# Kernel optimization log

Hardware: AMD Instinct MI355X
Metric: run time of the kernel (lower is better)

Reference implementation:

```python
import jax, jax.numpy as jnp
import numpy as np

N, E = 20000, 200000
DIM, EDGE_DIM, HID = 128, 64, 256


def _linear_init(key, fan_in, fan_out):
    # torch nn.Linear default: U(-1/sqrt(fan_in), 1/sqrt(fan_in)) for W and b
    kw, kb = jax.random.split(key)
    bound = 1.0 / np.sqrt(fan_in)
    W = jax.random.uniform(kw, (fan_in, fan_out), minval=-bound, maxval=bound, dtype=jnp.float32)
    b = jax.random.uniform(kb, (fan_out,), minval=-bound, maxval=bound, dtype=jnp.float32)
    return W, b


def setup_inputs() -> dict:
    key = jax.random.key(0)
    ks = jax.random.split(key, 8)
    H = jax.random.normal(ks[0], (N, DIM), dtype=jnp.float32)
    src = jax.random.randint(ks[1], (E,), 0, N, dtype=jnp.int32)
    dst = jax.random.randint(ks[2], (E,), 0, N, dtype=jnp.int32)
    edge_index = jnp.stack([src, dst], axis=0)
    edge_attr = jax.random.normal(ks[3], (E, EDGE_DIM), dtype=jnp.float32)
    msg_W1, msg_b1 = _linear_init(ks[4], DIM + EDGE_DIM, HID)
    msg_W2, msg_b2 = _linear_init(ks[5], HID, DIM)
    self_W1, self_b1 = _linear_init(ks[6], DIM, HID)
    self_W2, self_b2 = _linear_init(ks[7], HID, DIM)
    eps = jnp.zeros((1,), dtype=jnp.float32)
    return dict(H=H, edge_index=edge_index, edge_attr=edge_attr, eps=eps,
                msg_W1=msg_W1, msg_b1=msg_b1, msg_W2=msg_W2, msg_b2=msg_b2,
                self_W1=self_W1, self_b1=self_b1, self_W2=self_W2, self_b2=self_b2)


def _mlp(x, W1, b1, W2, b2):
    h = jax.nn.relu(x @ W1 + b1)
    return h @ W2 + b2


def reference(H, edge_index, edge_attr, eps,
              msg_W1, msg_b1, msg_W2, msg_b2,
              self_W1, self_b1, self_W2, self_b2):
    src, dst = edge_index[0], edge_index[1]
    # gather source node features, concat edge features -> per-edge message MLP
    msg_in = jnp.concatenate([H[src], edge_attr], axis=-1)  # [E, dim+edge_dim]
    msg = _mlp(msg_in, msg_W1, msg_b1, msg_W2, msg_b2)       # [E, dim]
    # scatter-add messages to destination nodes
    agg = jax.ops.segment_sum(msg, dst, num_segments=H.shape[0])  # [N, dim]
    return _mlp((1.0 + eps) * H + agg, self_W1, self_b1, self_W2, self_b2)
```

## Files before the change

kernel.cpp:

```cpp
#include <hip/hip_runtime.h>

typedef float  f32x4  __attribute__((ext_vector_type(4)));
typedef short  bf16x8 __attribute__((ext_vector_type(8)));
typedef unsigned short u16;

#define NN   20000
#define NE   200000
#define DIM  128
#define EDIM 64
#define HID  256
#define KIN  192

__device__ __forceinline__ u16 f2b(float f) {
  unsigned u = __float_as_uint(f);
  u += 0x7FFFu + ((u >> 16) & 1u);
  return (u16)(u >> 16);
}

__global__ void prep_kernel(const float* __restrict__ mW1, const float* __restrict__ mW2,
                            const float* __restrict__ sW1, const float* __restrict__ sW2,
                            u16* __restrict__ W1T, u16* __restrict__ W2T,
                            u16* __restrict__ S1T, u16* __restrict__ S2T) {
  int t  = blockIdx.x * blockDim.x + threadIdx.x;
  int nt = gridDim.x * blockDim.x;
  for (int i = t; i < KIN * HID; i += nt) { int k = i / HID, n = i % HID; W1T[n * KIN + k] = f2b(mW1[i]); }
  for (int i = t; i < HID * DIM; i += nt) { int k = i / DIM, n = i % DIM; W2T[n * HID + k] = f2b(mW2[i]); }
  for (int i = t; i < DIM * HID; i += nt) { int k = i / HID, n = i % HID; S1T[n * DIM + k] = f2b(sW1[i]); }
  for (int i = t; i < HID * DIM; i += nt) { int k = i / DIM, n = i % DIM; S2T[n * HID + k] = f2b(sW2[i]); }
}

__global__ __launch_bounds__(256) void edge_kernel(
    const float* __restrict__ H, const int* __restrict__ EI,
    const float* __restrict__ EA,
    const u16* __restrict__ W1T, const float* __restrict__ b1p,
    const u16* __restrict__ W2T, const float* __restrict__ b2p,
    float* __restrict__ agg) {
  __shared__ int src_s[64];
  __shared__ int dst_s[64];
  __shared__ u16 smem[64 * HID];

  const int tid = threadIdx.x;
  const int e0  = blockIdx.x * 64;
  if (tid < 64)       src_s[tid]      = EI[e0 + tid];
  else if (tid < 128) dst_s[tid - 64] = EI[NE + e0 + tid - 64];
  __syncthreads();

  #pragma unroll
  for (int i = 0; i < 8; ++i) {
    int idx = tid + i * 256;
    int row = idx >> 5, c4 = idx & 31;
    const float4 v = reinterpret_cast<const float4*>(H + (size_t)src_s[row] * DIM)[c4];
    int by = (c4 * 8) ^ ((row & 7) << 4);
    ushort4 o; o.x = f2b(v.x); o.y = f2b(v.y); o.z = f2b(v.z); o.w = f2b(v.w);
    *reinterpret_cast<ushort4*>(&smem[row * KIN + (by >> 1)]) = o;
  }
  #pragma unroll
  for (int i = 0; i < 4; ++i) {
    int idx = tid + i * 256;
    int row = idx >> 4, c4 = idx & 15;
    const float4 v = reinterpret_cast<const float4*>(EA + (size_t)(e0 + row) * EDIM)[c4];
    int by = (256 + c4 * 8) ^ ((row & 7) << 4);
    ushort4 o; o.x = f2b(v.x); o.y = f2b(v.y); o.z = f2b(v.z); o.w = f2b(v.w);
    *reinterpret_cast<ushort4*>(&smem[row * KIN + (by >> 1)]) = o;
  }
  __syncthreads();

  const int wv = tid >> 6, lane = tid & 63;
  const int lr = lane & 15, lg = lane >> 4;
  const f32x4 zero = {0.f, 0.f, 0.f, 0.f};

  const int n0 = wv * 64;
  f32x4 acc[4][4];
  #pragma unroll
  for (int m = 0; m < 4; ++m)
    #pragma unroll
    for (int n = 0; n < 4; ++n) acc[m][n] = zero;
  float bias1[4];
  #pragma unroll
  for (int n = 0; n < 4; ++n) bias1[n] = b1p[n0 + n * 16 + lr];

  #pragma unroll
  for (int kt = 0; kt < 6; ++kt) {
    bf16x8 af[4], bf[4];
    #pragma unroll
    for (int m = 0; m < 4; ++m) {
      int row = m * 16 + lr;
      int by  = (kt * 64 + lg * 16) ^ ((row & 7) << 4);
      af[m] = *reinterpret_cast<const bf16x8*>(&smem[row * KIN + (by >> 1)]);
    }
    #pragma unroll
    for (int n = 0; n < 4; ++n) {
      int nabs = n0 + n * 16 + lr;
      bf[n] = *reinterpret_cast<const bf16x8*>(&W1T[nabs * KIN + kt * 32 + lg * 8]);
    }
    #pragma unroll
    for (int m = 0; m < 4; ++m)
      #pragma unroll
      for (int n = 0; n < 4; ++n)
        acc[m][n] = __builtin_amdgcn_mfma_f32_16x16x32_bf16(af[m], bf[n], acc[m][n], 0, 0, 0);
  }
  __syncthreads();

  #pragma unroll
  for (int m = 0; m < 4; ++m)
    #pragma unroll
    for (int n = 0; n < 4; ++n)
      #pragma unroll
      for (int r = 0; r < 4; ++r) {
        int row = m * 16 + lg * 4 + r;
        int col = n0 + n * 16 + lr;
        float v = acc[m][n][r] + bias1[n];
        v = fmaxf(v, 0.0f);
        int by = (col * 2) ^ ((row & 7) << 4);
        smem[row * HID + (by >> 1)] = f2b(v);
      }
  __syncthreads();

  const int n0b = wv * 32;
  f32x4 acc2[4][2];
  #pragma unroll
  for (int m = 0; m < 4; ++m) { acc2[m][0] = zero; acc2[m][1] = zero; }
  float bias2[2];
  #pragma unroll
  for (int n = 0; n < 2; ++n) bias2[n] = b2p[n0b + n * 16 + lr];

  #pragma unroll
  for (int kt = 0; kt < 8; ++kt) {
    bf16x8 af[4], bf[2];
    #pragma unroll
    for (int m = 0; m < 4; ++m) {
      int row = m * 16 + lr;
      int by  = (kt * 64 + lg * 16) ^ ((row & 7) << 4);
      af[m] = *reinterpret_cast<const bf16x8*>(&smem[row * HID + (by >> 1)]);
    }
    #pragma unroll
    for (int n = 0; n < 2; ++n) {
      int nabs = n0b + n * 16 + lr;
      bf[n] = *reinterpret_cast<const bf16x8*>(&W2T[nabs * HID + kt * 32 + lg * 8]);
    }
    #pragma unroll
    for (int m = 0; m < 4; ++m)
      #pragma unroll
      for (int n = 0; n < 2; ++n)
        acc2[m][n] = __builtin_amdgcn_mfma_f32_16x16x32_bf16(af[m], bf[n], acc2[m][n], 0, 0, 0);
  }

  #pragma unroll
  for (int m = 0; m < 4; ++m)
    #pragma unroll
    for (int n = 0; n < 2; ++n) {
      int col = n0b + n * 16 + lr;
      float bb = bias2[n];
      #pragma unroll
      for (int r = 0; r < 4; ++r) {
        int row = m * 16 + lg * 4 + r;
        int d   = dst_s[row];
        atomicAdd(&agg[(size_t)d * DIM + col], acc2[m][n][r] + bb);
      }
    }
}

__global__ __launch_bounds__(256) void self_kernel(
    const float* __restrict__ H, const float* __restrict__ agg,
    const float* __restrict__ epsp,
    const u16* __restrict__ S1T, const float* __restrict__ b1p,
    const u16* __restrict__ S2T, const float* __restrict__ b2p,
    float* __restrict__ out) {
  __shared__ u16 smem[64 * HID];
  const int tid = threadIdx.x;
  const int r0  = blockIdx.x * 64;
  const float sc = 1.0f + epsp[0];

  #pragma unroll
  for (int i = 0; i < 8; ++i) {
    int idx = tid + i * 256;
    int row = idx >> 5, c4 = idx & 31;
    int gr = r0 + row; gr = gr < NN ? gr : NN - 1;
    const float4 h = reinterpret_cast<const float4*>(H   + (size_t)gr * DIM)[c4];
    const float4 a = reinterpret_cast<const float4*>(agg + (size_t)gr * DIM)[c4];
    ushort4 o;
    o.x = f2b(sc * h.x + a.x); o.y = f2b(sc * h.y + a.y);
    o.z = f2b(sc * h.z + a.z); o.w = f2b(sc * h.w + a.w);
    int by = (c4 * 8) ^ ((row & 7) << 4);
    *reinterpret_cast<ushort4*>(&smem[row * DIM + (by >> 1)]) = o;
  }
  __syncthreads();

  const int wv = tid >> 6, lane = tid & 63;
  const int lr = lane & 15, lg = lane >> 4;
  const f32x4 zero = {0.f, 0.f, 0.f, 0.f};

  const int n0 = wv * 64;
  f32x4 acc[4][4];
  #pragma unroll
  for (int m = 0; m < 4; ++m)
    #pragma unroll
    for (int n = 0; n < 4; ++n) acc[m][n] = zero;
  float bias1[4];
  #pragma unroll
  for (int n = 0; n < 4; ++n) bias1[n] = b1p[n0 + n * 16 + lr];

  #pragma unroll
  for (int kt = 0; kt < 4; ++kt) {
    bf16x8 af[4], bf[4];
    #pragma unroll
    for (int m = 0; m < 4; ++m) {
      int row = m * 16 + lr;
      int by  = (kt * 64 + lg * 16) ^ ((row & 7) << 4);
      af[m] = *reinterpret_cast<const bf16x8*>(&smem[row * DIM + (by >> 1)]);
    }
    #pragma unroll
    for (int n = 0; n < 4; ++n) {
      int nabs = n0 + n * 16 + lr;
      bf[n] = *reinterpret_cast<const bf16x8*>(&S1T[nabs * DIM + kt * 32 + lg * 8]);
    }
    #pragma unroll
    for (int m = 0; m < 4; ++m)
      #pragma unroll
      for (int n = 0; n < 4; ++n)
        acc[m][n] = __builtin_amdgcn_mfma_f32_16x16x32_bf16(af[m], bf[n], acc[m][n], 0, 0, 0);
  }
  __syncthreads();

  #pragma unroll
  for (int m = 0; m < 4; ++m)
    #pragma unroll
    for (int n = 0; n < 4; ++n)
      #pragma unroll
      for (int r = 0; r < 4; ++r) {
        int row = m * 16 + lg * 4 + r;
        int col = n0 + n * 16 + lr;
        float v = acc[m][n][r] + bias1[n];
        v = fmaxf(v, 0.0f);
        int by = (col * 2) ^ ((row & 7) << 4);
        smem[row * HID + (by >> 1)] = f2b(v);
      }
  __syncthreads();

  const int n0b = wv * 32;
  f32x4 acc2[4][2];
  #pragma unroll
  for (int m = 0; m < 4; ++m) { acc2[m][0] = zero; acc2[m][1] = zero; }
  float bias2[2];
  #pragma unroll
  for (int n = 0; n < 2; ++n) bias2[n] = b2p[n0b + n * 16 + lr];

  #pragma unroll
  for (int kt = 0; kt < 8; ++kt) {
    bf16x8 af[4], bf[2];
    #pragma unroll
    for (int m = 0; m < 4; ++m) {
      int row = m * 16 + lr;
      int by  = (kt * 64 + lg * 16) ^ ((row & 7) << 4);
      af[m] = *reinterpret_cast<const bf16x8*>(&smem[row * HID + (by >> 1)]);
    }
    #pragma unroll
    for (int n = 0; n < 2; ++n) {
      int nabs = n0b + n * 16 + lr;
      bf[n] = *reinterpret_cast<const bf16x8*>(&S2T[nabs * HID + kt * 32 + lg * 8]);
    }
    #pragma unroll
    for (int m = 0; m < 4; ++m)
      #pragma unroll
      for (int n = 0; n < 2; ++n)
        acc2[m][n] = __builtin_amdgcn_mfma_f32_16x16x32_bf16(af[m], bf[n], acc2[m][n], 0, 0, 0);
  }

  #pragma unroll
  for (int m = 0; m < 4; ++m)
    #pragma unroll
    for (int n = 0; n < 2; ++n) {
      int col = n0b + n * 16 + lr;
      float bb = bias2[n];
      #pragma unroll
      for (int r = 0; r < 4; ++r) {
        int row = m * 16 + lg * 4 + r;
        int gr  = r0 + row;
        if (gr < NN) out[(size_t)gr * DIM + col] = acc2[m][n][r] + bb;
      }
    }
}

extern "C" void kernel_launch(void* const* d_in, const int* in_sizes, int n_in,
                              void* d_out, int out_size, void* d_ws, size_t ws_size,
                              hipStream_t stream) {
  const float* H   = (const float*)d_in[0];
  const int*   EI  = (const int*)  d_in[1];
  const float* EA  = (const float*)d_in[2];
  const float* EPS = (const float*)d_in[3];
  const float* mW1 = (const float*)d_in[4];
  const float* mb1 = (const float*)d_in[5];
  const float* mW2 = (const float*)d_in[6];
  const float* mb2 = (const float*)d_in[7];
  const float* sW1 = (const float*)d_in[8];
  const float* sb1 = (const float*)d_in[9];
  const float* sW2 = (const float*)d_in[10];
  const float* sb2 = (const float*)d_in[11];
  float* out = (float*)d_out;

  char* ws = (char*)d_ws;
  float* agg = (float*)ws;
  size_t off = (size_t)NN * DIM * 4;
  u16* W1T = (u16*)(ws + off); off += (size_t)HID * KIN * 2;
  u16* W2T = (u16*)(ws + off); off += (size_t)DIM * HID * 2;
  u16* S1T = (u16*)(ws + off); off += (size_t)HID * DIM * 2;
  u16* S2T = (u16*)(ws + off); off += (size_t)DIM * HID * 2;

  hipMemsetAsync(agg, 0, (size_t)NN * DIM * 4, stream);
  prep_kernel<<<96, 256, 0, stream>>>(mW1, mW2, sW1, sW2, W1T, W2T, S1T, S2T);
  edge_kernel<<<NE / 64, 256, 0, stream>>>(H, EI, EA, W1T, mb1, W2T, mb2, agg);
  self_kernel<<<(NN + 63) / 64, 256, 0, stream>>>(H, agg, EPS, S1T, sb1, S2T, sb2, out);
}
```

Before: 244.5 us.

## Replace float atomic scatter with CSR-sorted bf16 messages and gather reduction

Builds a per-destination histogram and prefix scan so that each edge message gets a slot in a dst-sorted buffer. The edge kernel now writes bf16 messages into that buffer instead of issuing fp32 atomicAdds to agg. A new node kernel reduces each node's contiguous messages before running the self MLP, using 32-row tiles. This removes the 25.6M global float atomics and the agg memset. In exchange it adds two small kernels (one of them a single-block scan), a 51MB message buffer, and bf16 rounding of each message before summation.

```diff
diff --git a/kernel.cpp b/kernel.cpp
--- a/kernel.cpp
+++ b/kernel.cpp
@@ -15,6 +15,9 @@
   unsigned u = __float_as_uint(f);
   u += 0x7FFFu + ((u >> 16) & 1u);
   return (u16)(u >> 16);
+}
+__device__ __forceinline__ float b2f(u16 v) {
+  return __uint_as_float(((unsigned)v) << 16);
 }
 
 __global__ void prep_kernel(const float* __restrict__ mW1, const float* __restrict__ mW2,
@@ -29,20 +32,58 @@
   for (int i = t; i < HID * DIM; i += nt) { int k = i / DIM, n = i % DIM; S2T[n * HID + k] = f2b(sW2[i]); }
 }
 
-__global__ __launch_bounds__(256) void edge_kernel(
+__global__ void hist_kernel(const int* __restrict__ EI, int* __restrict__ cnt) {
+  int i = blockIdx.x * 256 + threadIdx.x;
+  if (i < NE) atomicAdd(&cnt[EI[NE + i]], 1);
+}
+
+__global__ __launch_bounds__(1024) void scan_kernel(const int* __restrict__ cnt,
+                                                    int* __restrict__ start,
+                                                    int* __restrict__ cursor) {
+  __shared__ int ls[1024];
+  const int t = threadIdx.x;
+  const int base = t * 20;
+  int v[20]; int s = 0;
+  #pragma unroll
+  for (int j = 0; j < 20; ++j) {
+    int idx = base + j;
+    int c = (idx < NN) ? cnt[idx] : 0;
+    v[j] = s; s += c;
+  }
+  ls[t] = s;
+  __syncthreads();
+  for (int off = 1; off < 1024; off <<= 1) {
+    int x = (t >= off) ? ls[t - off] : 0;
+    __syncthreads();
+    ls[t] += x;
+    __syncthreads();
+  }
+  int boff = (t > 0) ? ls[t - 1] : 0;
+  #pragma unroll
+  for (int j = 0; j < 20; ++j) {
+    int idx = base + j;
+    if (idx < NN) { int val = boff + v[j]; start[idx] = val; cursor[idx] = val; }
+  }
+  if (t == 0) start[NN] = NE;
+}
+
+__global__ __launch_bounds__(256, 4) void edge_kernel(
     const float* __restrict__ H, const int* __restrict__ EI,
     const float* __restrict__ EA,
     const u16* __restrict__ W1T, const float* __restrict__ b1p,
     const u16* __restrict__ W2T, const float* __restrict__ b2p,
-    float* __restrict__ agg) {
+    int* __restrict__ cursor, u16* __restrict__ msg) {
   __shared__ int src_s[64];
-  __shared__ int dst_s[64];
+  __shared__ int pos_s[64];
   __shared__ u16 smem[64 * HID];
 
   const int tid = threadIdx.x;
   const int e0  = blockIdx.x * 64;
-  if (tid < 64)       src_s[tid]      = EI[e0 + tid];
-  else if (tid < 128) dst_s[tid - 64] = EI[NE + e0 + tid - 64];
+  if (tid < 64) {
+    int e = e0 + tid;
+    src_s[tid] = EI[e];
+    pos_s[tid] = atomicAdd(&cursor[EI[NE + e]], 1);
+  }
   __syncthreads();
 
   #pragma unroll
@@ -154,35 +195,57 @@
       #pragma unroll
       for (int r = 0; r < 4; ++r) {
         int row = m * 16 + lg * 4 + r;
-        int d   = dst_s[row];
-        atomicAdd(&agg[(size_t)d * DIM + col], acc2[m][n][r] + bb);
-      }
-    }
-}
-
-__global__ __launch_bounds__(256) void self_kernel(
-    const float* __restrict__ H, const float* __restrict__ agg,
-    const float* __restrict__ epsp,
+        msg[(size_t)pos_s[row] * DIM + col] = f2b(acc2[m][n][r] + bb);
+      }
+    }
+}
+
+__global__ __launch_bounds__(256, 6) void node_kernel(
+    const float* __restrict__ H, const u16* __restrict__ msg,
+    const int* __restrict__ start_g, const float* __restrict__ epsp,
     const u16* __restrict__ S1T, const float* __restrict__ b1p,
     const u16* __restrict__ S2T, const float* __restrict__ b2p,
     float* __restrict__ out) {
-  __shared__ u16 smem[64 * HID];
+  __shared__ int start_s[33];
+  __shared__ u16 smem[32 * HID];
   const int tid = threadIdx.x;
-  const int r0  = blockIdx.x * 64;
+  const int r0  = blockIdx.x * 32;
   const float sc = 1.0f + epsp[0];
 
-  #pragma unroll
-  for (int i = 0; i < 8; ++i) {
-    int idx = tid + i * 256;
-    int row = idx >> 5, c4 = idx & 31;
-    int gr = r0 + row; gr = gr < NN ? gr : NN - 1;
-    const float4 h = reinterpret_cast<const float4*>(H   + (size_t)gr * DIM)[c4];
-    const float4 a = reinterpret_cast<const float4*>(agg + (size_t)gr * DIM)[c4];
-    ushort4 o;
-    o.x = f2b(sc * h.x + a.x); o.y = f2b(sc * h.y + a.y);
-    o.z = f2b(sc * h.z + a.z); o.w = f2b(sc * h.w + a.w);
-    int by = (c4 * 8) ^ ((row & 7) << 4);
-    *reinterpret_cast<ushort4*>(&smem[row * DIM + (by >> 1)]) = o;
+  if (tid < 33) start_s[tid] = start_g[r0 + tid];
+  __syncthreads();
+
+  {
+    const int node = tid >> 3;
+    const int c0   = (tid & 7) * 16;
+    float a[16];
+    #pragma unroll
+    for (int j = 0; j < 16; ++j) a[j] = 0.f;
+    const int s0 = start_s[node], s1 = start_s[node + 1];
+    for (int i = s0; i < s1; ++i) {
+      const u16* rp = msg + (size_t)i * DIM + c0;
+      bf16x8 lo = *reinterpret_cast<const bf16x8*>(rp);
+      bf16x8 hi = *reinterpret_cast<const bf16x8*>(rp + 8);
+      #pragma unroll
+      for (int j = 0; j < 8; ++j) {
+        a[j]     += b2f((u16)lo[j]);
+        a[8 + j] += b2f((u16)hi[j]);
+      }
+    }
+    const int gr = r0 + node;
+    const float4* hp = reinterpret_cast<const float4*>(H + (size_t)gr * DIM + c0);
+    #pragma unroll
+    for (int q = 0; q < 4; ++q) {
+      float4 h = hp[q];
+      ushort4 o;
+      o.x = f2b(sc * h.x + a[q * 4 + 0]);
+      o.y = f2b(sc * h.y + a[q * 4 + 1]);
+      o.z = f2b(sc * h.z + a[q * 4 + 2]);
+      o.w = f2b(sc * h.w + a[q * 4 + 3]);
+      int col = c0 + q * 4;
+      int by = (col * 2) ^ ((node & 7) << 4);
+      *reinterpret_cast<ushort4*>(&smem[node * DIM + (by >> 1)]) = o;
+    }
   }
   __syncthreads();
 
@@ -191,9 +254,9 @@
   const f32x4 zero = {0.f, 0.f, 0.f, 0.f};
 
   const int n0 = wv * 64;
-  f32x4 acc[4][4];
-  #pragma unroll
-  for (int m = 0; m < 4; ++m)
+  f32x4 acc[2][4];
+  #pragma unroll
+  for (int m = 0; m < 2; ++m)
     #pragma unroll
     for (int n = 0; n < 4; ++n) acc[m][n] = zero;
   float bias1[4];
@@ -202,9 +265,9 @@
 
   #pragma unroll
   for (int kt = 0; kt < 4; ++kt) {
-    bf16x8 af[4], bf[4];
-    #pragma unroll
-    for (int m = 0; m < 4; ++m) {
+    bf16x8 af[2], bf[4];
+    #pragma unroll
+    for (int m = 0; m < 2; ++m) {
       int row = m * 16 + lr;
       int by  = (kt * 64 + lg * 16) ^ ((row & 7) << 4);
       af[m] = *reinterpret_cast<const bf16x8*>(&smem[row * DIM + (by >> 1)]);
@@ -215,7 +278,7 @@
       bf[n] = *reinterpret_cast<const bf16x8*>(&S1T[nabs * DIM + kt * 32 + lg * 8]);
     }
     #pragma unroll
-    for (int m = 0; m < 4; ++m)
+    for (int m = 0; m < 2; ++m)
       #pragma unroll
       for (int n = 0; n < 4; ++n)
         acc[m][n] = __builtin_amdgcn_mfma_f32_16x16x32_bf16(af[m], bf[n], acc[m][n], 0, 0, 0);
@@ -223,7 +286,7 @@
   __syncthreads();
 
   #pragma unroll
-  for (int m = 0; m < 4; ++m)
+  for (int m = 0; m < 2; ++m)
     #pragma unroll
     for (int n = 0; n < 4; ++n)
       #pragma unroll
@@ -238,18 +301,18 @@
   __syncthreads();
 
   const int n0b = wv * 32;
-  f32x4 acc2[4][2];
-  #pragma unroll
-  for (int m = 0; m < 4; ++m) { acc2[m][0] = zero; acc2[m][1] = zero; }
+  f32x4 acc2[2][2];
+  #pragma unroll
+  for (int m = 0; m < 2; ++m) { acc2[m][0] = zero; acc2[m][1] = zero; }
   float bias2[2];
   #pragma unroll
   for (int n = 0; n < 2; ++n) bias2[n] = b2p[n0b + n * 16 + lr];
 
   #pragma unroll
   for (int kt = 0; kt < 8; ++kt) {
-    bf16x8 af[4], bf[2];
-    #pragma unroll
-    for (int m = 0; m < 4; ++m) {
+    bf16x8 af[2], bf[2];
+    #pragma unroll
+    for (int m = 0; m < 2; ++m) {
       int row = m * 16 + lr;
       int by  = (kt * 64 + lg * 16) ^ ((row & 7) << 4);
       af[m] = *reinterpret_cast<const bf16x8*>(&smem[row * HID + (by >> 1)]);
@@ -260,14 +323,14 @@
       bf[n] = *reinterpret_cast<const bf16x8*>(&S2T[nabs * HID + kt * 32 + lg * 8]);
     }
     #pragma unroll
-    for (int m = 0; m < 4; ++m)
+    for (int m = 0; m < 2; ++m)
       #pragma unroll
       for (int n = 0; n < 2; ++n)
         acc2[m][n] = __builtin_amdgcn_mfma_f32_16x16x32_bf16(af[m], bf[n], acc2[m][n], 0, 0, 0);
   }
 
   #pragma unroll
-  for (int m = 0; m < 4; ++m)
+  for (int m = 0; m < 2; ++m)
     #pragma unroll
     for (int n = 0; n < 2; ++n) {
       int col = n0b + n * 16 + lr;
@@ -276,7 +339,7 @@
       for (int r = 0; r < 4; ++r) {
         int row = m * 16 + lg * 4 + r;
         int gr  = r0 + row;
-        if (gr < NN) out[(size_t)gr * DIM + col] = acc2[m][n][r] + bb;
+        out[(size_t)gr * DIM + col] = acc2[m][n][r] + bb;
       }
     }
 }
@@ -299,15 +362,21 @@
   float* out = (float*)d_out;
 
   char* ws = (char*)d_ws;
-  float* agg = (float*)ws;
-  size_t off = (size_t)NN * DIM * 4;
+  size_t off = 0;
+  int* cnt    = (int*)(ws + off); off += (size_t)NN * 4;
+  int* start  = (int*)(ws + off); off += (size_t)(NN + 1) * 4;
+  int* cursor = (int*)(ws + off); off += (size_t)NN * 4;
   u16* W1T = (u16*)(ws + off); off += (size_t)HID * KIN * 2;
   u16* W2T = (u16*)(ws + off); off += (size_t)DIM * HID * 2;
   u16* S1T = (u16*)(ws + off); off += (size_t)HID * DIM * 2;
   u16* S2T = (u16*)(ws + off); off += (size_t)DIM * HID * 2;
-
-  hipMemsetAsync(agg, 0, (size_t)NN * DIM * 4, stream);
+  off = (off + 511) & ~(size_t)511;
+  u16* msg = (u16*)(ws + off); off += (size_t)NE * DIM * 2;
+
+  hipMemsetAsync(cnt, 0, (size_t)NN * 4, stream);
   prep_kernel<<<96, 256, 0, stream>>>(mW1, mW2, sW1, sW2, W1T, W2T, S1T, S2T);
-  edge_kernel<<<NE / 64, 256, 0, stream>>>(H, EI, EA, W1T, mb1, W2T, mb2, agg);
-  self_kernel<<<(NN + 63) / 64, 256, 0, stream>>>(H, agg, EPS, S1T, sb1, S2T, sb2, out);
-}
+  hist_kernel<<<(NE + 255) / 256, 256, 0, stream>>>(EI, cnt);
+  scan_kernel<<<1, 1024, 0, stream>>>(cnt, start, cursor);
+  edge_kernel<<<NE / 64, 256, 0, stream>>>(H, EI, EA, W1T, mb1, W2T, mb2, cursor, msg);
+  node_kernel<<<NN / 32, 256, 0, stream>>>(H, msg, start, EPS, S1T, sb1, S2T, sb2, out);
+}
```

Measured after the change: 253.4 us. 3.7% more time.
